# Kernel optimization log

Hardware: AMD Instinct MI355X
Metric: run time of the kernel (lower is better)

## Reference

```python
import jax, jax.numpy as jnp
import numpy as np
import math

B, L, D_MODEL = 8, 1024, 512
D_INNER = 1024          # expand*d_model
D2 = D_INNER // 2       # per-branch channels
DT_RANK = 32            # ceil(d_model/16)
D_STATE = 16
K = 4                   # d_conv
HIDDEN = 4 * D_MODEL


def setup_inputs() -> dict:
    key = jax.random.key(0)
    ks = jax.random.split(key, 12)
    rn = lambda k, s, sc: jax.random.normal(k, s, jnp.float32) * sc
    x = rn(ks[0], (B, L, D_MODEL), 1.0)
    in_proj_w = rn(ks[1], (D_INNER, D_MODEL), D_MODEL ** -0.5)
    conv_x_w = rn(ks[2], (D2, 1, K), 0.2)
    conv_z_w = rn(ks[3], (D2, 1, K), 0.2)
    x_proj_w = rn(ks[4], (DT_RANK + 2 * D_STATE, D2), D2 ** -0.5)
    dt_proj_w = rn(ks[5], (D2, DT_RANK), DT_RANK ** -0.5)
    dt = jnp.exp(jax.random.uniform(ks[6], (D2,)) * (math.log(0.1) - math.log(0.001)) + math.log(0.001))
    dt_proj_b = dt + jnp.log(-jnp.expm1(-dt))  # inverse softplus
    A_log = jnp.log(jnp.tile(jnp.arange(1, D_STATE + 1, dtype=jnp.float32)[None, :], (D2, 1)))
    ssm_D = jnp.ones((D2,), jnp.float32)
    out_proj_w = rn(ks[7], (D_MODEL, D_INNER), D_INNER ** -0.5)
    fc1_w = rn(ks[8], (HIDDEN, D_MODEL), D_MODEL ** -0.5)
    fc2_w = rn(ks[9], (D_MODEL, HIDDEN), HIDDEN ** -0.5)
    return dict(x=x,
                ln1_w=jnp.ones((D_MODEL,)), ln1_b=jnp.zeros((D_MODEL,)),
                in_proj_w=in_proj_w, conv_x_w=conv_x_w, conv_z_w=conv_z_w,
                x_proj_w=x_proj_w, dt_proj_w=dt_proj_w, dt_proj_b=dt_proj_b,
                A_log=A_log, ssm_D=ssm_D, out_proj_w=out_proj_w,
                ln2_w=jnp.ones((D_MODEL,)), ln2_b=jnp.zeros((D_MODEL,)),
                fc1_w=fc1_w, fc1_b=jnp.zeros((HIDDEN,)),
                fc2_w=fc2_w, fc2_b=jnp.zeros((D_MODEL,)))


def _layernorm(x, w, b, eps=1e-5):
    m = jnp.mean(x, -1, keepdims=True)
    v = jnp.mean((x - m) ** 2, -1, keepdims=True)
    return (x - m) * jax.lax.rsqrt(v + eps) * w + b


def _dwconv1d_same(x, w):
    # x: (b, c, l); w: (c, 1, K). torch 'same' for even K pads (left=1, right=2)
    return jax.lax.conv_general_dilated(
        x, w, window_strides=(1,), padding=[(1, 2)],
        dimension_numbers=('NCH', 'OIH', 'NCH'), feature_group_count=x.shape[1])


def _selective_scan(u, delta, A, Bc, Cc, Dp):
    # u, delta: (b, d, l); A: (d, n); Bc, Cc: (b, n, l); Dp: (d,)
    dA = jnp.exp(delta[..., None] * A[None, :, None, :])            # (b,d,l,n)
    Bt = jnp.moveaxis(Bc, 2, 1)                                     # (b,l,n)
    dBu = (delta * u)[..., None] * Bt[:, None, :, :]                # (b,d,l,n)
    dA_l = jnp.moveaxis(dA, 2, 0)                                   # (l,b,d,n)
    dBu_l = jnp.moveaxis(dBu, 2, 0)

    def step(h, t):
        dAt, dBut = t
        h = dAt * h + dBut
        return h, h

    h0 = jnp.zeros((u.shape[0], u.shape[1], A.shape[1]), u.dtype)
    _, hs = jax.lax.scan(step, h0, (dA_l, dBu_l))                   # hs: (l,b,d,n)
    Ct = jnp.moveaxis(Cc, 2, 0)                                     # (l,b,n)
    y = jnp.einsum('lbdn,lbn->bdl', hs, Ct)
    return y + Dp[None, :, None] * u


def _mixer(xn, in_proj_w, conv_x_w, conv_z_w, x_proj_w, dt_proj_w, dt_proj_b, A_log, ssm_D, out_proj_w):
    # xn: (b, l, d_model)
    xz = jnp.einsum('bld,ed->bel', xn, in_proj_w)                   # (b, d_inner, l)
    xh, zh = jnp.split(xz, 2, axis=1)                               # (b, d2, l) each
    xh = jax.nn.silu(_dwconv1d_same(xh, conv_x_w))
    zh = jax.nn.silu(_dwconv1d_same(zh, conv_z_w))
    x_dbl = jnp.einsum('bdl,rd->brl', xh, x_proj_w)                 # (b, R+2n, l)
    dt, Bc, Cc = jnp.split(x_dbl, [DT_RANK, DT_RANK + D_STATE], axis=1)
    dt = jnp.einsum('brl,dr->bdl', dt, dt_proj_w)
    delta = jax.nn.softplus(dt + dt_proj_b[None, :, None])          # delta_bias + delta_softplus
    A = -jnp.exp(A_log)
    y = _selective_scan(xh, delta, A, Bc, Cc, ssm_D)                # (b, d2, l)
    out = jnp.concatenate([y, zh], axis=1)                          # (b, d_inner, l)
    return jnp.einsum('bdl,ed->ble', out, out_proj_w)               # (b, l, d_model)


def reference(x, ln1_w, ln1_b, in_proj_w, conv_x_w, conv_z_w, x_proj_w, dt_proj_w, dt_proj_b,
              A_log, ssm_D, out_proj_w, ln2_w, ln2_b, fc1_w, fc1_b, fc2_w, fc2_b):
    h = x + _mixer(_layernorm(x, ln1_w, ln1_b), in_proj_w, conv_x_w, conv_z_w,
                   x_proj_w, dt_proj_w, dt_proj_b, A_log, ssm_D, out_proj_w)
    h2 = _layernorm(h, ln2_w, ln2_b)
    mlp = jax.nn.gelu(h2 @ fc1_w.T + fc1_b, approximate=False) @ fc2_w.T + fc2_b
    return h + mlp
```

## Files before the change

### kernel.cpp

```cpp
#include <hip/hip_runtime.h>
#include <stdint.h>


#define MROWS 8192
#define LSEQ 1024
#define DMODEL 512
#define DINNER 1024
#define D2 512
#define NSTATE 16
#define HIDDEN 2048
#define NCHUNK 16
#define LCHUNK 64

typedef unsigned short us;
typedef short short8 __attribute__((ext_vector_type(8)));
typedef float floatx4 __attribute__((ext_vector_type(4)));

__device__ __forceinline__ us f2bf(float f) {
    unsigned int u = __float_as_uint(f);
    u = (u + 0x7fffu + ((u >> 16) & 1u)) >> 16;
    return (us)u;
}
__device__ __forceinline__ float bf2f(us u) {
    return __uint_as_float(((unsigned int)u) << 16);
}

__device__ __forceinline__ void g2lds16(const void* g, void* l) {
    typedef __attribute__((address_space(1))) void GV;
    typedef __attribute__((address_space(3))) void LV;
    GV* gp = (GV*)(uintptr_t)g;
    LV* lp = (LV*)(uint32_t)(uintptr_t)l;
    __builtin_amdgcn_global_load_lds(gp, lp, 16, 0, 0);
}

__device__ __forceinline__ void pack_slot(const float* __restrict__ w,
                                          us* __restrict__ dst, int K, int sig)
{
    int lane = sig & 63;
    int KS = K >> 5;
    int ks = (sig >> 6) % KS;
    int g = sig / (KS << 6);
    const float* src = w + (size_t)(g * 16 + (lane & 15)) * K
                         + ks * 32 + (lane >> 4) * 8;
    short8 o;
    #pragma unroll
    for (int e = 0; e < 8; e++) o[e] = (short)f2bf(src[e]);
    *(short8*)(dst + (size_t)sig * 8) = o;
}

__global__ __launch_bounds__(256) void cvt_pack6(
    const float* __restrict__ w0, const float* __restrict__ w1,
    const float* __restrict__ w2, const float* __restrict__ w3,
    const float* __restrict__ w4, const float* __restrict__ w5,
    us* __restrict__ o0, us* __restrict__ o1, us* __restrict__ o2,
    us* __restrict__ o3, us* __restrict__ o4, us* __restrict__ o5)
{
    int bx = blockIdx.x, t = threadIdx.x;
    if (bx < 256)        pack_slot(w0, o0, 512,  bx * 256 + t);
    else if (bx < 272)   pack_slot(w1, o1, 512,  (bx - 256) * 256 + t);
    else if (bx < 280)   pack_slot(w2, o2, 32,   (bx - 272) * 256 + t);
    else if (bx < 536)   pack_slot(w3, o3, 1024, (bx - 280) * 256 + t);
    else if (bx < 1048)  pack_slot(w4, o4, 512,  (bx - 536) * 256 + t);
    else                 pack_slot(w5, o5, 2048, (bx - 1048) * 256 + t);
}

__global__ __launch_bounds__(256) void ln_pack(
    const float* __restrict__ x, const float* __restrict__ w,
    const float* __restrict__ b, us* __restrict__ outp)
{
    int g = blockIdx.x, t = threadIdx.x;
    __shared__ float T[16][516];
    __shared__ float mu[16], rs[16];
    const float* src = x + (size_t)g * 16 * DMODEL;
    #pragma unroll
    for (int p = 0; p < 8; p++) {
        int idx4 = p * 256 + t;
        int row = idx4 >> 7, c = (idx4 & 127) << 2;
        float4 v = *(const float4*)(src + (size_t)row * DMODEL + c);
        *(float4*)&T[row][c] = v;
    }
    __syncthreads();
    int r = t >> 4, i = t & 15;
    float s = 0.f, ss = 0.f;
    #pragma unroll
    for (int c = 0; c < 32; c++) {
        float v = T[r][c * 16 + i];
        s += v; ss += v * v;
    }
    #pragma unroll
    for (int off = 8; off > 0; off >>= 1) {
        s += __shfl_down(s, off, 16);
        ss += __shfl_down(ss, off, 16);
    }
    if (i == 0) {
        float m = s * (1.f / DMODEL);
        mu[r] = m;
        rs[r] = rsqrtf(ss * (1.f / DMODEL) - m * m + 1e-5f);
    }
    __syncthreads();
    #pragma unroll
    for (int s0 = 0; s0 < 4; s0++) {
        int sig = t * 4 + s0;
        int lane = sig & 63, ks = sig >> 6;
        int lr = lane & 15, lq = lane >> 4;
        int k0 = ks * 32 + lq * 8;
        float m = mu[lr], r2 = rs[lr];
        short8 o;
        #pragma unroll
        for (int e = 0; e < 8; e++)
            o[e] = (short)f2bf((T[lr][k0 + e] - m) * r2 * w[k0 + e] + b[k0 + e]);
        *(short8*)(outp + (size_t)g * 8192 + sig * 8) = o;
    }
}

#define MO_ROWBF16 0
#define MO_F32_PACK 1
#define MO_SOFTPLUS 2
#define MO_RES 3
#define MO_GELU_PACK 4
#define MO_BIAS_RES 5

template <int MODE, int BN>
__global__ __launch_bounds__(256) void gemm_pk(
    const us* __restrict__ Ap, int KA,
    const us* __restrict__ Bp, int KB, int Kloop,
    int Nout, int ldc,
    float* __restrict__ outF, us* __restrict__ outB, us* __restrict__ outP,
    const float* __restrict__ bias, const float* __restrict__ res)
{
    constexpr int NBg = BN / 16;
    constexpr int NJ = BN / 32;
    constexpr int TS = 4 + NBg;
    constexpr int PS = TS / 4;
    constexpr int SMSZ = 64 * (BN + 4) * 4;
    __shared__ __align__(16) char smraw[SMSZ];
    us* sA = (us*)smraw;
    us* sB = sA + 2048;
    float (*TT)[BN + 4] = (float (*)[BN + 4])smraw;

    int t = threadIdx.x;
    int lane = t & 63, w = t >> 6;
    int lr = lane & 15, lq = lane >> 4;
    int m0 = blockIdx.x * 64, n0 = blockIdx.y * BN;
    int gA0 = blockIdx.x * 4;
    int gB0 = n0 >> 4;

    floatx4 acc[2][NJ];
    #pragma unroll
    for (int i = 0; i < 2; i++)
        #pragma unroll
        for (int j = 0; j < NJ; j++) acc[i][j] = (floatx4){0.f, 0.f, 0.f, 0.f};

    for (int ks = 0; ks * 32 < Kloop; ks++) {
        #pragma unroll
        for (int s = 0; s < PS; s++) {
            int slot = w * PS + s;
            if (slot < 4)
                g2lds16(Ap + ((size_t)(gA0 + slot) * KA + ks * 32) * 16 + lane * 8,
                        sA + slot * 512);
            else
                g2lds16(Bp + ((size_t)(gB0 + slot - 4) * KB + ks * 32) * 16 + lane * 8,
                        sB + (slot - 4) * 512);
        }
        __syncthreads();
        short8 af[2], bfv[NJ];
        #pragma unroll
        for (int i = 0; i < 2; i++)
            af[i] = *(const short8*)(sA + ((w & 1) * 2 + i) * 512 + lane * 8);
        #pragma unroll
        for (int j = 0; j < NJ; j++)
            bfv[j] = *(const short8*)(sB + ((w >> 1) * NJ + j) * 512 + lane * 8);
        #pragma unroll
        for (int i = 0; i < 2; i++)
            #pragma unroll
            for (int j = 0; j < NJ; j++)
                acc[i][j] = __builtin_amdgcn_mfma_f32_16x16x32_bf16(
                    af[i], bfv[j], acc[i][j], 0, 0, 0);
        __syncthreads();
    }

    #pragma unroll
    for (int i = 0; i < 2; i++)
        #pragma unroll
        for (int j = 0; j < NJ; j++)
            #pragma unroll
            for (int r = 0; r < 4; r++)
                TT[(w & 1) * 32 + i * 16 + lq * 4 + r]
                  [(w >> 1) * (BN / 2) + j * 16 + lr] = acc[i][j][r];
    __syncthreads();

    if (MODE == MO_F32_PACK || MODE == MO_SOFTPLUS || MODE == MO_RES ||
        MODE == MO_BIAS_RES) {
        constexpr int passes = 64 * BN / 4 / 256;
        #pragma unroll
        for (int p = 0; p < passes; p++) {
            int idx = p * 256 + t;
            int row = idx / (BN / 4);
            int c = (idx % (BN / 4)) * 4;
            float4 v = *(float4*)&TT[row][c];
            int col = n0 + c;
            size_t o = (size_t)(m0 + row) * ldc + col;
            float4 rv = {0, 0, 0, 0}, bv = {0, 0, 0, 0};
            if (MODE == MO_RES || MODE == MO_BIAS_RES) rv = *(const float4*)(res + o);
            if (MODE == MO_SOFTPLUS || MODE == MO_BIAS_RES) bv = *(const float4*)(bias + col);
            float vv[4] = {v.x, v.y, v.z, v.w};
            float rr[4] = {rv.x, rv.y, rv.z, rv.w};
            float bb[4] = {bv.x, bv.y, bv.z, bv.w};
            float oo[4];
            #pragma unroll
            for (int e = 0; e < 4; e++) {
                if (MODE == MO_SOFTPLUS) {
                    float tb = vv[e] + bb[e];
                    oo[e] = (tb > 20.f) ? tb : log1pf(__expf(tb));
                } else if (MODE == MO_RES) {
                    oo[e] = vv[e] + rr[e];
                } else if (MODE == MO_BIAS_RES) {
                    oo[e] = vv[e] + bb[e] + rr[e];
                } else {
                    oo[e] = vv[e];
                }
            }
            float4 ov = {oo[0], oo[1], oo[2], oo[3]};
            *(float4*)(outF + o) = ov;
        }
    }
    if (MODE == MO_ROWBF16) {
        constexpr int passes = 64 * BN / 8 / 256;
        #pragma unroll
        for (int p = 0; p < passes; p++) {
            int idx = p * 256 + t;
            int row = idx / (BN / 8);
            int c = (idx % (BN / 8)) * 8;
            short8 o8;
            #pragma unroll
            for (int e = 0; e < 8; e++) o8[e] = (short)f2bf(TT[row][c + e]);
            *(short8*)(outB + (size_t)(m0 + row) * ldc + n0 + c) = o8;
        }
    }
    if (MODE == MO_F32_PACK || MODE == MO_GELU_PACK) {
        constexpr int passes = 8 * BN / 256;
        #pragma unroll
        for (int p = 0; p < passes; p++) {
            int sig = p * 256 + t;
            int gi = sig / (2 * BN);
            int rem = sig % (2 * BN);
            int ksl = rem >> 6;
            int ln2 = rem & 63;
            int lr2 = ln2 & 15, lq2 = ln2 >> 4;
            int mloc = gi * 16 + lr2;
            int nloc = ksl * 32 + lq2 * 8;
            short8 o8;
            #pragma unroll
            for (int e = 0; e < 8; e++) {
                float vv = TT[mloc][nloc + e];
                if (MODE == MO_GELU_PACK) {
                    float tb = vv + bias[n0 + nloc + e];
                    vv = 0.5f * tb * (1.f + erff(tb * 0.70710678118f));
                }
                o8[e] = (short)f2bf(vv);
            }
            *(short8*)(outP + ((size_t)((m0 >> 4) + gi) * Nout + n0 + ksl * 32) * 16
                       + ln2 * 8) = o8;
        }
    }
}

__global__ __launch_bounds__(256) void conv_pk(
    const us* __restrict__ xz, const float* __restrict__ cwx,
    const float* __restrict__ cwz, float* __restrict__ xh_f,
    us* __restrict__ xh_p, us* __restrict__ outbuf_p)
{
    int bx = blockIdx.x, t = threadIdx.x;
    int b = bx >> 6, g = bx & 63;
    size_t rowbase = (size_t)b * LSEQ;
    #pragma unroll
    for (int s = 0; s < 4; s++) {
        int sig = t * 4 + s;
        int ks = sig >> 6, lane = sig & 63;
        int lr = lane & 15, lq = lane >> 4;
        int l = g * 16 + lr;
        int d0 = ks * 32 + lq * 8;
        float ax[8] = {0, 0, 0, 0, 0, 0, 0, 0};
        #pragma unroll
        for (int kk = 0; kk < 4; kk++) {
            int ls = l + kk - 1;
            if (ls >= 0 && ls < LSEQ) {
                const us* src = xz + (rowbase + ls) * DINNER + d0;
                #pragma unroll
                for (int e = 0; e < 8; e++)
                    ax[e] += cwx[(d0 + e) * 4 + kk] * bf2f(src[e]);
            }
        }
        short8 o8;
        float vo[8];
        #pragma unroll
        for (int e = 0; e < 8; e++) {
            float v = ax[e];
            v = v / (1.f + __expf(-v));
            vo[e] = v;
            o8[e] = (short)f2bf(v);
        }
        *(short8*)(xh_p + (size_t)bx * 8192 + sig * 8) = o8;
        float* fo = xh_f + (rowbase + l) * D2 + d0;
        float4 f0 = {vo[0], vo[1], vo[2], vo[3]};
        float4 f1 = {vo[4], vo[5], vo[6], vo[7]};
        *(float4*)fo = f0;
        *(float4*)(fo + 4) = f1;
    }
    #pragma unroll
    for (int s = 0; s < 4; s++) {
        int sig = t * 4 + s;
        int ks = sig >> 6, lane = sig & 63;
        int lr = lane & 15, lq = lane >> 4;
        int l = g * 16 + lr;
        int d0 = ks * 32 + lq * 8;
        float az[8] = {0, 0, 0, 0, 0, 0, 0, 0};
        #pragma unroll
        for (int kk = 0; kk < 4; kk++) {
            int ls = l + kk - 1;
            if (ls >= 0 && ls < LSEQ) {
                const us* src = xz + (rowbase + ls) * DINNER + 512 + d0;
                #pragma unroll
                for (int e = 0; e < 8; e++)
                    az[e] += cwz[(d0 + e) * 4 + kk] * bf2f(src[e]);
            }
        }
        short8 o8;
        #pragma unroll
        for (int e = 0; e < 8; e++) {
            float v = az[e];
            v = v / (1.f + __expf(-v));
            o8[e] = (short)f2bf(v);
        }
        *(short8*)(outbuf_p + (size_t)bx * 16384 + 8192 + sig * 8) = o8;
    }
}

__global__ __launch_bounds__(256) void scan_phase1(
    const float* __restrict__ delta, const float* __restrict__ u,
    const float* __restrict__ xdbl, const float* __restrict__ A_log,
    float* __restrict__ S, float* __restrict__ P)
{
    int bx = blockIdx.x;
    int b = bx >> 5, rem = bx & 31, c = rem >> 1, half = rem & 1;
    int d = half * 256 + threadIdx.x;
    float A[NSTATE], h[NSTATE];
    #pragma unroll
    for (int n = 0; n < NSTATE; n++) {
        A[n] = -__expf(A_log[d * NSTATE + n]);
        h[n] = 0.f;
    }
    float sdt = 0.f;
    int l0 = c * LCHUNK;
    for (int l = l0; l < l0 + LCHUNK; ++l) {
        size_t idx = (size_t)(b * LSEQ + l);
        float dv = delta[idx * D2 + d];
        float uv = u[idx * D2 + d];
        float du = dv * uv;
        const float4* Bp = (const float4*)(xdbl + idx * 64 + 32);
        float4 B0 = Bp[0], B1 = Bp[1], B2 = Bp[2], B3 = Bp[3];
        float Bn[16] = {B0.x, B0.y, B0.z, B0.w, B1.x, B1.y, B1.z, B1.w,
                        B2.x, B2.y, B2.z, B2.w, B3.x, B3.y, B3.z, B3.w};
        sdt += dv;
        #pragma unroll
        for (int n = 0; n < NSTATE; n++)
            h[n] = __expf(dv * A[n]) * h[n] + du * Bn[n];
    }
    size_t o = ((size_t)(b * D2 + d)) * (NCHUNK * NSTATE) + c * NSTATE;
    #pragma unroll
    for (int n = 0; n < NSTATE; n++) {
        S[o + n] = h[n];
        P[o + n] = __expf(sdt * A[n]);
    }
}

__global__ __launch_bounds__(256) void scan_phase2(
    const float* __restrict__ S, const float* __restrict__ P,
    float* __restrict__ hin)
{
    int gid = blockIdx.x * 256 + threadIdx.x;
    int n = gid & 15;
    size_t base = ((size_t)(gid >> 4)) * (NCHUNK * NSTATE) + n;
    float h = 0.f;
    for (int c = 0; c < NCHUNK; c++) {
        size_t o = base + c * NSTATE;
        hin[o] = h;
        h = P[o] * h + S[o];
    }
}

__global__ __launch_bounds__(256) void scan_phase3(
    const float* __restrict__ delta, const float* __restrict__ u,
    const float* __restrict__ xdbl, const float* __restrict__ hin,
    const float* __restrict__ A_log, const float* __restrict__ Dvec,
    us* __restrict__ outbuf_p)
{
    int bx = blockIdx.x;
    int b = bx >> 5, rem = bx & 31, c = rem >> 1, half = rem & 1;
    int t = threadIdx.x;
    int d = half * 256 + t;
    __shared__ us yl[64][264];
    float A[NSTATE], h[NSTATE];
    size_t hb = ((size_t)(b * D2 + d)) * (NCHUNK * NSTATE) + c * NSTATE;
    #pragma unroll
    for (int n = 0; n < NSTATE; n++) {
        A[n] = -__expf(A_log[d * NSTATE + n]);
        h[n] = hin[hb + n];
    }
    float Dd = Dvec[d];
    int l0 = c * LCHUNK;
    for (int l = l0; l < l0 + LCHUNK; ++l) {
        size_t idx = (size_t)(b * LSEQ + l);
        float dv = delta[idx * D2 + d];
        float uv = u[idx * D2 + d];
        float du = dv * uv;
        const float4* Bp = (const float4*)(xdbl + idx * 64 + 32);
        const float4* Cp = (const float4*)(xdbl + idx * 64 + 48);
        float4 B0 = Bp[0], B1 = Bp[1], B2 = Bp[2], B3 = Bp[3];
        float4 C0 = Cp[0], C1 = Cp[1], C2 = Cp[2], C3 = Cp[3];
        float Bn[16] = {B0.x, B0.y, B0.z, B0.w, B1.x, B1.y, B1.z, B1.w,
                        B2.x, B2.y, B2.z, B2.w, B3.x, B3.y, B3.z, B3.w};
        float Cn[16] = {C0.x, C0.y, C0.z, C0.w, C1.x, C1.y, C1.z, C1.w,
                        C2.x, C2.y, C2.z, C2.w, C3.x, C3.y, C3.z, C3.w};
        float y = Dd * uv;
        #pragma unroll
        for (int n = 0; n < NSTATE; n++) {
            h[n] = __expf(dv * A[n]) * h[n] + du * Bn[n];
            y += h[n] * Cn[n];
        }
        yl[l - l0][t] = f2bf(y);
    }
    __syncthreads();
    int g0 = (b * LSEQ + l0) >> 4;
    #pragma unroll
    for (int s = 0; s < 8; s++) {
        int sig = t * 8 + s;
        int gi = sig >> 9;
        int rem2 = sig & 511;
        int ksl = rem2 >> 6;
        int lane = rem2 & 63;
        int lr = lane & 15, lq = lane >> 4;
        uint4 v = *(uint4*)&yl[gi * 16 + lr][ksl * 32 + lq * 8];
        *(uint4*)(outbuf_p + ((size_t)(g0 + gi) * 1024 + (half * 8 + ksl) * 32) * 16
                  + lane * 8) = v;
    }
}

extern "C" void kernel_launch(void* const* d_in, const int* in_sizes, int n_in,
                              void* d_out, int out_size, void* d_ws, size_t ws_size,
                              hipStream_t stream)
{
    const float* x         = (const float*)d_in[0];
    const float* ln1_w     = (const float*)d_in[1];
    const float* ln1_b     = (const float*)d_in[2];
    const float* in_proj_w = (const float*)d_in[3];
    const float* conv_x_w  = (const float*)d_in[4];
    const float* conv_z_w  = (const float*)d_in[5];
    const float* x_proj_w  = (const float*)d_in[6];
    const float* dt_proj_w = (const float*)d_in[7];
    const float* dt_proj_b = (const float*)d_in[8];
    const float* A_log     = (const float*)d_in[9];
    const float* ssm_D     = (const float*)d_in[10];
    const float* out_proj_w= (const float*)d_in[11];
    const float* ln2_w     = (const float*)d_in[12];
    const float* ln2_b     = (const float*)d_in[13];
    const float* fc1_w     = (const float*)d_in[14];
    const float* fc1_b     = (const float*)d_in[15];
    const float* fc2_w     = (const float*)d_in[16];
    const float* fc2_b     = (const float*)d_in[17];
    float* out = (float*)d_out;

    char* p = (char*)d_ws;
    us* wp_in  = (us*)(p);
    us* wp_x   = (us*)(p + 1048576);
    us* wp_dt  = (us*)(p + 1114112);
    us* wp_out = (us*)(p + 1146880);
    us* wp_f1  = (us*)(p + 2195456);
    us* wp_f2  = (us*)(p + 4292608);
    us*    xn_p    = (us*)(p + 6389760);
    us*    xz      = (us*)(p + 14778368);
    us*    xh_p    = (us*)(p + 31555584);
    float* xh_f    = (float*)(p + 39944192);
    us*    outbuf_p= (us*)(p + 56721408);
    float* xdbl_f  = (float*)(p + 73498624);
    us*    xdbl_p  = (us*)(p + 75595776);
    float* delta_f = (float*)(p + 76644352);
    float* scanS   = (float*)(p + 93421568);
    float* scanP   = (float*)(p + 97615872);
    float* hin     = (float*)(p + 101810176);
    float* h_f     = (float*)(p + 106004480);
    us*    h2_p    = xn_p;
    us*    mlp1_p  = xz;

    cvt_pack6<<<1560, 256, 0, stream>>>(in_proj_w, x_proj_w, dt_proj_w,
        out_proj_w, fc1_w, fc2_w, wp_in, wp_x, wp_dt, wp_out, wp_f1, wp_f2);

    ln_pack<<<512, 256, 0, stream>>>(x, ln1_w, ln1_b, xn_p);

    gemm_pk<MO_ROWBF16, 128><<<dim3(128, 8), 256, 0, stream>>>(
        xn_p, 512, wp_in, 512, 512, 0, DINNER,
        nullptr, xz, nullptr, nullptr, nullptr);

    conv_pk<<<512, 256, 0, stream>>>(xz, conv_x_w, conv_z_w, xh_f, xh_p, outbuf_p);

    gemm_pk<MO_F32_PACK, 64><<<dim3(128, 1), 256, 0, stream>>>(
        xh_p, 512, wp_x, 512, 512, 64, 64,
        xdbl_f, nullptr, xdbl_p, nullptr, nullptr);

    gemm_pk<MO_SOFTPLUS, 64><<<dim3(128, 8), 256, 0, stream>>>(
        xdbl_p, 64, wp_dt, 32, 32, 0, D2,
        delta_f, nullptr, nullptr, dt_proj_b, nullptr);

    scan_phase1<<<256, 256, 0, stream>>>(delta_f, xh_f, xdbl_f, A_log, scanS, scanP);
    scan_phase2<<<256, 256, 0, stream>>>(scanS, scanP, hin);
    scan_phase3<<<512, 256, 0, stream>>>(delta_f, xh_f, xdbl_f, hin, A_log,
        ssm_D, outbuf_p);

    gemm_pk<MO_RES, 64><<<dim3(128, 8), 256, 0, stream>>>(
        outbuf_p, 1024, wp_out, 1024, 1024, 0, DMODEL,
        h_f, nullptr, nullptr, nullptr, x);

    ln_pack<<<512, 256, 0, stream>>>(h_f, ln2_w, ln2_b, h2_p);

    gemm_pk<MO_GELU_PACK, 128><<<dim3(128, 16), 256, 0, stream>>>(
        h2_p, 512, wp_f1, 512, 512, 2048, HIDDEN,
        nullptr, nullptr, mlp1_p, fc1_b, nullptr);

    gemm_pk<MO_BIAS_RES, 64><<<dim3(128, 8), 256, 0, stream>>>(
        mlp1_p, 2048, wp_f2, 2048, 2048, 0, DMODEL,
        out, nullptr, nullptr, fc2_b, h_f);
}
```

Baseline: 366.1 us.

## Add 128x128-tile GEMM staging weights in LDS for the four large projections

Adds a new GEMM kernel with 128x128 output tiles. It stages 256-wide K slabs of the packed weight matrix into LDS and streams the pre-packed A fragments directly from global memory with register double-buffering. The in_proj, out_proj, fc1 and fc2 GEMMs switch to it with fewer, larger blocks, aiming for more weight reuse and fewer LDS round-trips per MFMA. The trade-off is a 64KB LDS buffer that limits blocks per CU, and grids as small as 256 blocks for the N=512 GEMMs, which may underfill the device.

Result: slower. 457.0 us (+24.8%).

```diff
diff --git a/kernel.cpp b/kernel.cpp
--- a/kernel.cpp
+++ b/kernel.cpp
@@ -120,6 +120,130 @@
 #define MO_GELU_PACK 4
 #define MO_BIAS_RES 5
 
+template <int MODE>
+__global__ __launch_bounds__(256, 2) void gemm_wlds(
+    const us* __restrict__ Ap, const us* __restrict__ Bp, int K,
+    int Nout, int ldc,
+    float* __restrict__ outF, us* __restrict__ outB, us* __restrict__ outP,
+    const float* __restrict__ bias, const float* __restrict__ res)
+{
+    __shared__ __align__(16) us sW[32768];
+    int t = threadIdx.x;
+    int lane = t & 63, w = t >> 6;
+    int lr = lane & 15, lq = lane >> 4;
+    int m0 = blockIdx.x * 128, n0 = blockIdx.y * 128;
+    int gB0 = blockIdx.y * 8;
+    const int NK = K >> 8;
+
+    floatx4 acc[2][8];
+    #pragma unroll
+    for (int i = 0; i < 2; i++)
+        #pragma unroll
+        for (int j = 0; j < 8; j++) acc[i][j] = (floatx4){0.f, 0.f, 0.f, 0.f};
+
+    const us* Abase0 = Ap + ((size_t)(blockIdx.x * 8 + w * 2) * K) * 16 + lane * 8;
+    const us* Abase1 = Abase0 + (size_t)K * 16;
+
+    for (int ph = 0; ph < NK; ph++) {
+        #pragma unroll
+        for (int s = 0; s < 16; s++) {
+            int slot = w * 16 + s;
+            int j = slot >> 3, kl = slot & 7;
+            g2lds16(Bp + ((size_t)(gB0 + j) * K + ph * 256 + kl * 32) * 16 + lane * 8,
+                    sW + slot * 512);
+        }
+        __syncthreads();
+
+        short8 afb[2][2];
+        afb[0][0] = *(const short8*)(Abase0 + (size_t)ph * 4096);
+        afb[0][1] = *(const short8*)(Abase1 + (size_t)ph * 4096);
+        #pragma unroll
+        for (int kl = 0; kl < 8; kl++) {
+            if (kl < 7) {
+                afb[(kl + 1) & 1][0] =
+                    *(const short8*)(Abase0 + (size_t)ph * 4096 + (kl + 1) * 512);
+                afb[(kl + 1) & 1][1] =
+                    *(const short8*)(Abase1 + (size_t)ph * 4096 + (kl + 1) * 512);
+            }
+            short8 bf[8];
+            #pragma unroll
+            for (int j = 0; j < 8; j++)
+                bf[j] = *(const short8*)(sW + (j * 8 + kl) * 512 + lane * 8);
+            #pragma unroll
+            for (int i = 0; i < 2; i++)
+                #pragma unroll
+                for (int j = 0; j < 8; j++)
+                    acc[i][j] = __builtin_amdgcn_mfma_f32_16x16x32_bf16(
+                        afb[kl & 1][i], bf[j], acc[i][j], 0, 0, 0);
+        }
+        __syncthreads();
+    }
+
+    float (*TT)[128] = (float (*)[128])sW;
+    #pragma unroll
+    for (int i = 0; i < 2; i++)
+        #pragma unroll
+        for (int j = 0; j < 8; j++)
+            #pragma unroll
+            for (int r = 0; r < 4; r++)
+                TT[w * 32 + i * 16 + lq * 4 + r][j * 16 + lr] = acc[i][j][r];
+    __syncthreads();
+
+    if (MODE == MO_ROWBF16) {
+        #pragma unroll
+        for (int p = 0; p < 8; p++) {
+            int idx = p * 256 + t;
+            int row = idx >> 4, c = (idx & 15) << 3;
+            short8 o8;
+            #pragma unroll
+            for (int e = 0; e < 8; e++) o8[e] = (short)f2bf(TT[row][c + e]);
+            *(short8*)(outB + (size_t)(m0 + row) * ldc + n0 + c) = o8;
+        }
+    }
+    if (MODE == MO_RES || MODE == MO_BIAS_RES) {
+        #pragma unroll
+        for (int p = 0; p < 16; p++) {
+            int idx = p * 256 + t;
+            int row = idx >> 5, c = (idx & 31) << 2;
+            float4 v = *(float4*)&TT[row][c];
+            int col = n0 + c;
+            size_t o = (size_t)(m0 + row) * ldc + col;
+            float4 rv = *(const float4*)(res + o);
+            float4 ov;
+            if (MODE == MO_BIAS_RES) {
+                float4 bv = *(const float4*)(bias + col);
+                ov.x = v.x + bv.x + rv.x; ov.y = v.y + bv.y + rv.y;
+                ov.z = v.z + bv.z + rv.z; ov.w = v.w + bv.w + rv.w;
+            } else {
+                ov.x = v.x + rv.x; ov.y = v.y + rv.y;
+                ov.z = v.z + rv.z; ov.w = v.w + rv.w;
+            }
+            *(float4*)(outF + o) = ov;
+        }
+    }
+    if (MODE == MO_GELU_PACK) {
+        #pragma unroll
+        for (int p = 0; p < 8; p++) {
+            int sig = p * 256 + t;
+            int gi = sig >> 8;
+            int rem = sig & 255;
+            int ksl = rem >> 6;
+            int ln2 = rem & 63;
+            int lr2 = ln2 & 15, lq2 = ln2 >> 4;
+            short8 o8;
+            #pragma unroll
+            for (int e = 0; e < 8; e++) {
+                int colg = n0 + ksl * 32 + lq2 * 8 + e;
+                float tb = TT[gi * 16 + lr2][ksl * 32 + lq2 * 8 + e] + bias[colg];
+                float vv = 0.5f * tb * (1.f + erff(tb * 0.70710678118f));
+                o8[e] = (short)f2bf(vv);
+            }
+            *(short8*)(outP + ((size_t)((m0 >> 4) + gi) * Nout + n0 + ksl * 32) * 16
+                       + ln2 * 8) = o8;
+        }
+    }
+}
+
 template <int MODE, int BN>
 __global__ __launch_bounds__(256) void gemm_pk(
     const us* __restrict__ Ap, int KA,
@@ -189,8 +313,7 @@
                   [(w >> 1) * (BN / 2) + j * 16 + lr] = acc[i][j][r];
     __syncthreads();
 
-    if (MODE == MO_F32_PACK || MODE == MO_SOFTPLUS || MODE == MO_RES ||
-        MODE == MO_BIAS_RES) {
+    if (MODE == MO_F32_PACK || MODE == MO_SOFTPLUS) {
         constexpr int passes = 64 * BN / 4 / 256;
         #pragma unroll
         for (int p = 0; p < passes; p++) {
@@ -200,22 +323,13 @@
             float4 v = *(float4*)&TT[row][c];
             int col = n0 + c;
             size_t o = (size_t)(m0 + row) * ldc + col;
-            float4 rv = {0, 0, 0, 0}, bv = {0, 0, 0, 0};
-            if (MODE == MO_RES || MODE == MO_BIAS_RES) rv = *(const float4*)(res + o);
-            if (MODE == MO_SOFTPLUS || MODE == MO_BIAS_RES) bv = *(const float4*)(bias + col);
             float vv[4] = {v.x, v.y, v.z, v.w};
-            float rr[4] = {rv.x, rv.y, rv.z, rv.w};
-            float bb[4] = {bv.x, bv.y, bv.z, bv.w};
             float oo[4];
             #pragma unroll
             for (int e = 0; e < 4; e++) {
                 if (MODE == MO_SOFTPLUS) {
-                    float tb = vv[e] + bb[e];
+                    float tb = vv[e] + bias[col + e];
                     oo[e] = (tb > 20.f) ? tb : log1pf(__expf(tb));
-                } else if (MODE == MO_RES) {
-                    oo[e] = vv[e] + rr[e];
-                } else if (MODE == MO_BIAS_RES) {
-                    oo[e] = vv[e] + bb[e] + rr[e];
                 } else {
                     oo[e] = vv[e];
                 }
@@ -224,20 +338,7 @@
             *(float4*)(outF + o) = ov;
         }
     }
-    if (MODE == MO_ROWBF16) {
-        constexpr int passes = 64 * BN / 8 / 256;
-        #pragma unroll
-        for (int p = 0; p < passes; p++) {
-            int idx = p * 256 + t;
-            int row = idx / (BN / 8);
-            int c = (idx % (BN / 8)) * 8;
-            short8 o8;
-            #pragma unroll
-            for (int e = 0; e < 8; e++) o8[e] = (short)f2bf(TT[row][c + e]);
-            *(short8*)(outB + (size_t)(m0 + row) * ldc + n0 + c) = o8;
-        }
-    }
-    if (MODE == MO_F32_PACK || MODE == MO_GELU_PACK) {
+    if (MODE == MO_F32_PACK) {
         constexpr int passes = 8 * BN / 256;
         #pragma unroll
         for (int p = 0; p < passes; p++) {
@@ -247,18 +348,10 @@
             int ksl = rem >> 6;
             int ln2 = rem & 63;
             int lr2 = ln2 & 15, lq2 = ln2 >> 4;
-            int mloc = gi * 16 + lr2;
-            int nloc = ksl * 32 + lq2 * 8;
             short8 o8;
             #pragma unroll
-            for (int e = 0; e < 8; e++) {
-                float vv = TT[mloc][nloc + e];
-                if (MODE == MO_GELU_PACK) {
-                    float tb = vv + bias[n0 + nloc + e];
-                    vv = 0.5f * tb * (1.f + erff(tb * 0.70710678118f));
-                }
-                o8[e] = (short)f2bf(vv);
-            }
+            for (int e = 0; e < 8; e++)
+                o8[e] = (short)f2bf(TT[gi * 16 + lr2][ksl * 32 + lq2 * 8 + e]);
             *(short8*)(outP + ((size_t)((m0 >> 4) + gi) * Nout + n0 + ksl * 32) * 16
                        + ln2 * 8) = o8;
         }
@@ -497,9 +590,8 @@
 
     ln_pack<<<512, 256, 0, stream>>>(x, ln1_w, ln1_b, xn_p);
 
-    gemm_pk<MO_ROWBF16, 128><<<dim3(128, 8), 256, 0, stream>>>(
-        xn_p, 512, wp_in, 512, 512, 0, DINNER,
-        nullptr, xz, nullptr, nullptr, nullptr);
+    gemm_wlds<MO_ROWBF16><<<dim3(64, 8), 256, 0, stream>>>(
+        xn_p, wp_in, 512, 0, DINNER, nullptr, xz, nullptr, nullptr, nullptr);
 
     conv_pk<<<512, 256, 0, stream>>>(xz, conv_x_w, conv_z_w, xh_f, xh_p, outbuf_p);
 
@@ -516,17 +608,14 @@
     scan_phase3<<<512, 256, 0, stream>>>(delta_f, xh_f, xdbl_f, hin, A_log,
         ssm_D, outbuf_p);
 
-    gemm_pk<MO_RES, 64><<<dim3(128, 8), 256, 0, stream>>>(
-        outbuf_p, 1024, wp_out, 1024, 1024, 0, DMODEL,
-        h_f, nullptr, nullptr, nullptr, x);
+    gemm_wlds<MO_RES><<<dim3(64, 4), 256, 0, stream>>>(
+        outbuf_p, wp_out, 1024, 0, DMODEL, h_f, nullptr, nullptr, nullptr, x);
 
     ln_pack<<<512, 256, 0, stream>>>(h_f, ln2_w, ln2_b, h2_p);
 
-    gemm_pk<MO_GELU_PACK, 128><<<dim3(128, 16), 256, 0, stream>>>(
-        h2_p, 512, wp_f1, 512, 512, 2048, HIDDEN,
-        nullptr, nullptr, mlp1_p, fc1_b, nullptr);
-
-    gemm_pk<MO_BIAS_RES, 64><<<dim3(128, 8), 256, 0, stream>>>(
-        mlp1_p, 2048, wp_f2, 2048, 2048, 0, DMODEL,
-        out, nullptr, nullptr, fc2_b, h_f);
-}
+    gemm_wlds<MO_GELU_PACK><<<dim3(64, 16), 256, 0, stream>>>(
+        h2_p, wp_f1, 512, HIDDEN, 0, nullptr, nullptr, mlp1_p, fc1_b, nullptr);
+
+    gemm_wlds<MO_BIAS_RES><<<dim3(64, 4), 256, 0, stream>>>(
+        mlp1_p, wp_f2, 2048, 0, DMODEL, out, nullptr, nullptr, fc2_b, h_f);
+}
```
